# Optimization experiments

Hardware: AMD Instinct MI355X
Metric: run time of the kernel (lower is better)

## Reference

```python
import jax, jax.numpy as jnp
import numpy as np

B, L, H, D = 64, 2048, 1024, 128  # segments, segment length, hidden, input_dim
N = B * L

def swish(z):
    return z * jax.nn.sigmoid(z)

def setup_inputs() -> dict:
    key = jax.random.key(0)
    ks = jax.random.split(key, 10)
    s = 0.02
    x_seeds = jax.random.normal(ks[0], (N, D), dtype=jnp.float32)
    x_nodes = jax.random.normal(ks[1], (N, D), dtype=jnp.float32)
    W_seed = jax.random.normal(ks[2], (H, D), dtype=jnp.float32) * s
    W_node = jax.random.normal(ks[3], (H, D), dtype=jnp.float32) * s
    W1 = jax.random.normal(ks[4], (H, H), dtype=jnp.float32) * s
    b1 = jnp.zeros((H,), dtype=jnp.float32)
    W2 = jax.random.normal(ks[5], (H, H), dtype=jnp.float32) * s
    b2 = jnp.zeros((H,), dtype=jnp.float32)
    w_ns = jax.random.normal(ks[6], (1, H), dtype=jnp.float32) * s   # node_score_layer (zero-init in src; random for nontrivial baseline)
    W_stop = jax.random.normal(ks[7], (2, H), dtype=jnp.float32) * s  # stopping_score_layer
    starts = jnp.arange(B, dtype=jnp.int32) * L
    indptr = jnp.stack([starts, starts + L, starts + L], axis=1)  # (start, end, candidate_end)
    return {"x_seeds": x_seeds, "x_nodes": x_nodes, "W_seed": W_seed, "W_node": W_node,
            "W1": W1, "b1": b1, "W2": W2, "b2": b2, "w_ns": w_ns, "W_stop": W_stop,
            "indptr": indptr}

def reference(x_seeds, x_nodes, W_seed, W_node, W1, b1, W2, b2, w_ns, W_stop, indptr):
    # embeddings + 2-layer Swish MLP
    h = x_seeds @ W_seed.T + x_nodes @ W_node.T            # [N, H]
    h = swish(h @ W1.T + b1)
    h = swish(h @ W2.T + b2)
    node_scores = (h @ w_ns.T)[:, 0]                       # [N]
    # ragged segments (uniform length L) defined by indptr starts
    nb = indptr.shape[0]
    seg_len = h.shape[0] // nb                             # static L
    idx = indptr[:, 0][:, None] + jnp.arange(seg_len)      # [B, L]
    h_seg = h[idx]                                         # [B, L, H]
    stop_node = h_seg.mean(axis=1)                         # [B, H] per-segment mean pool
    node_logits = jax.nn.log_softmax(node_scores[idx], axis=1)          # [B, L]
    stop_logits = jax.nn.log_softmax(stop_node @ W_stop.T, axis=1)      # [B, 2]
    # concat([node_logits + stop0, stop1]) per segment
    return jnp.concatenate([node_logits + stop_logits[:, :1], stop_logits[:, 1:]], axis=1)  # [B, L+1]
```

## Files before the change

kernel.cpp:

```cpp
#include <hip/hip_runtime.h>

typedef float f32x4 __attribute__((ext_vector_type(4)));
typedef __bf16 bf16x8 __attribute__((ext_vector_type(8)));
typedef unsigned short u16x8 __attribute__((ext_vector_type(8)));

#define DEVINL static __device__ __forceinline__

DEVINL unsigned short f2bf(float f) {
    unsigned int u = __builtin_bit_cast(unsigned int, f);
    u += 0x7fffu + ((u >> 16) & 1u);
    return (unsigned short)(u >> 16);
}
DEVINL float bf2f(unsigned short u) {
    unsigned int x = ((unsigned int)u) << 16;
    return __builtin_bit_cast(float, x);
}

#define GLD16(gp, lp)                                                          \
    __builtin_amdgcn_global_load_lds(                                          \
        (const __attribute__((address_space(1))) void*)(gp),                   \
        (__attribute__((address_space(3))) void*)(lp), 16, 0, 0)

__global__ void pack_cat_k(const float* __restrict__ s0, const float* __restrict__ s1,
                           unsigned short* __restrict__ dst, int nchunks) {
    int e = blockIdx.x * 256 + threadIdx.x;
    if (e >= nchunks) return;
    int row = e >> 5, ch = e & 31;
    const float* src = (ch < 16) ? (s0 + (size_t)row * 128 + ch * 8)
                                 : (s1 + (size_t)row * 128 + (ch - 16) * 8);
    float4 a = *(const float4*)src;
    float4 b = *(const float4*)(src + 4);
    u16x8 o;
    o[0] = f2bf(a.x); o[1] = f2bf(a.y); o[2] = f2bf(a.z); o[3] = f2bf(a.w);
    o[4] = f2bf(b.x); o[5] = f2bf(b.y); o[6] = f2bf(b.z); o[7] = f2bf(b.w);
    *(u16x8*)(dst + (size_t)e * 8) = o;
}

__global__ void cvt_k(const float* __restrict__ s, unsigned short* __restrict__ d, int nchunks) {
    int e = blockIdx.x * 256 + threadIdx.x;
    if (e >= nchunks) return;
    float4 a = *(const float4*)(s + (size_t)e * 8);
    float4 b = *(const float4*)(s + (size_t)e * 8 + 4);
    u16x8 o;
    o[0] = f2bf(a.x); o[1] = f2bf(a.y); o[2] = f2bf(a.z); o[3] = f2bf(a.w);
    o[4] = f2bf(b.x); o[5] = f2bf(b.y); o[6] = f2bf(b.z); o[7] = f2bf(b.w);
    *(u16x8*)(d + (size_t)e * 8) = o;
}

template <int EPI>
__global__ void gemm_bt_k(const unsigned short* __restrict__ A,
                          const unsigned short* __restrict__ B,
                          const float* __restrict__ bias,
                          unsigned short* __restrict__ C,
                          int M, int N, int K) {
    __shared__ unsigned short As[128 * 32];
    __shared__ unsigned short Bs[128 * 32];
    const int tid  = threadIdx.x;
    const int lane = tid & 63;
    const int wv   = tid >> 6;
    const int wr   = wv >> 1, wc = wv & 1;
    const int ntn  = N >> 7;
    const int im   = blockIdx.x / ntn, in = blockIdx.x % ntn;
    const size_t rowA0 = (size_t)im * 128, rowB0 = (size_t)in * 128;

    const int e0 = tid, e1 = tid + 256;
    const int ra0 = e0 >> 2, ca0 = (e0 & 3) * 8;
    const int ra1 = e1 >> 2, ca1 = (e1 & 3) * 8;

    f32x4 acc[4][4] = {};

    const int frow = lane & 15;
    const int kb   = (lane >> 4) * 8;

    for (int k0 = 0; k0 < K; k0 += 32) {
        GLD16(A + (rowA0 + ra0) * K + k0 + ca0, (char*)As + e0 * 16);
        GLD16(A + (rowA0 + ra1) * K + k0 + ca1, (char*)As + e1 * 16);
        GLD16(B + (rowB0 + ra0) * K + k0 + ca0, (char*)Bs + e0 * 16);
        GLD16(B + (rowB0 + ra1) * K + k0 + ca1, (char*)Bs + e1 * 16);
        __syncthreads();

        bf16x8 af[4], bfr[4];
#pragma unroll
        for (int m = 0; m < 4; ++m)
            af[m] = *(const bf16x8*)&As[(wr * 64 + m * 16 + frow) * 32 + kb];
#pragma unroll
        for (int n = 0; n < 4; ++n)
            bfr[n] = *(const bf16x8*)&Bs[(wc * 64 + n * 16 + frow) * 32 + kb];
#pragma unroll
        for (int m = 0; m < 4; ++m)
#pragma unroll
            for (int n = 0; n < 4; ++n)
                acc[m][n] = __builtin_amdgcn_mfma_f32_16x16x32_bf16(af[m], bfr[n], acc[m][n], 0, 0, 0);
        __syncthreads();
    }

    const int r4 = (lane >> 4) * 4;
    const int cc = lane & 15;
#pragma unroll
    for (int n = 0; n < 4; ++n) {
        const int col = (int)rowB0 + wc * 64 + n * 16 + cc;
        const float bv = (EPI == 1) ? bias[col] : 0.0f;
#pragma unroll
        for (int m = 0; m < 4; ++m) {
            const size_t row = rowA0 + wr * 64 + m * 16 + r4;
#pragma unroll
            for (int r = 0; r < 4; ++r) {
                float v = acc[m][n][r] + bv;
                if (EPI == 1) v = v / (1.0f + __expf(-v));
                C[(row + r) * (size_t)N + col] = f2bf(v);
            }
        }
    }
}

__global__ void scores_k(const unsigned short* __restrict__ h,
                         const float* __restrict__ wns, float* __restrict__ sc) {
    const int lane = threadIdx.x & 63, wv = threadIdx.x >> 6;
    const size_t row = (size_t)blockIdx.x * 4 + wv;
    const unsigned short* p = h + row * 1024;
    float s = 0.f;
#pragma unroll
    for (int it = 0; it < 2; ++it) {
        const int base = (it * 64 + lane) * 8;
        u16x8 v = *(const u16x8*)&p[base];
        const float4 w0 = *(const float4*)&wns[base];
        const float4 w1 = *(const float4*)&wns[base + 4];
        s += bf2f(v[0]) * w0.x + bf2f(v[1]) * w0.y + bf2f(v[2]) * w0.z + bf2f(v[3]) * w0.w
           + bf2f(v[4]) * w1.x + bf2f(v[5]) * w1.y + bf2f(v[6]) * w1.z + bf2f(v[7]) * w1.w;
    }
#pragma unroll
    for (int off = 32; off; off >>= 1) s += __shfl_down(s, off);
    if (lane == 0) sc[row] = s;
}

__global__ void pool_k(const unsigned short* __restrict__ h, float* __restrict__ pool) {
    const int bi = blockIdx.x;
    const int b = bi >> 5, sub = bi & 31;
    const int rb = sub >> 2, cb = sub & 3;
    const int hc = cb * 256 + threadIdx.x;
    const unsigned short* p = h + ((size_t)b * 2048 + rb * 256) * 1024 + hc;
    float acc = 0.f;
#pragma unroll 8
    for (int r = 0; r < 256; ++r) acc += bf2f(p[(size_t)r * 1024]);
    atomicAdd(&pool[b * 1024 + hc], acc * (1.0f / 2048.0f));
}

__global__ void stop_k(const float* __restrict__ pool, const float* __restrict__ Wstop,
                       float* __restrict__ stp, float* __restrict__ out) {
    const int b = blockIdx.x, t = threadIdx.x;
    float a0 = 0.f, a1 = 0.f;
#pragma unroll
    for (int j = 0; j < 4; ++j) {
        const int hcol = t + j * 256;
        const float pv = pool[b * 1024 + hcol];
        a0 += pv * Wstop[hcol];
        a1 += pv * Wstop[1024 + hcol];
    }
    const int lane = t & 63, wv = t >> 6;
#pragma unroll
    for (int off = 32; off; off >>= 1) { a0 += __shfl_down(a0, off); a1 += __shfl_down(a1, off); }
    __shared__ float r0[4], r1[4];
    if (lane == 0) { r0[wv] = a0; r1[wv] = a1; }
    __syncthreads();
    if (t == 0) {
        const float s0 = r0[0] + r0[1] + r0[2] + r0[3];
        const float s1 = r1[0] + r1[1] + r1[2] + r1[3];
        const float m  = fmaxf(s0, s1);
        const float lse = m + __logf(__expf(s0 - m) + __expf(s1 - m));
        stp[b * 2] = s0 - lse;
        out[(size_t)b * 2049 + 2048] = s1 - lse;
    }
}

__global__ void node_k(const float* __restrict__ sc, const float* __restrict__ stp,
                       float* __restrict__ out) {
    const int b = blockIdx.x, t = threadIdx.x;
    const float* s = sc + (size_t)b * 2048;
    float v[8];
    float mx = -3.4e38f;
#pragma unroll
    for (int j = 0; j < 8; ++j) { v[j] = s[t + j * 256]; mx = fmaxf(mx, v[j]); }
    const int lane = t & 63, wv = t >> 6;
    __shared__ float red[4];
#pragma unroll
    for (int off = 32; off; off >>= 1) mx = fmaxf(mx, __shfl_down(mx, off));
    if (lane == 0) red[wv] = mx;
    __syncthreads();
    mx = fmaxf(fmaxf(red[0], red[1]), fmaxf(red[2], red[3]));
    float se = 0.f;
#pragma unroll
    for (int j = 0; j < 8; ++j) se += __expf(v[j] - mx);
    __syncthreads();
#pragma unroll
    for (int off = 32; off; off >>= 1) se += __shfl_down(se, off);
    if (lane == 0) red[wv] = se;
    __syncthreads();
    se = red[0] + red[1] + red[2] + red[3];
    const float base = stp[b * 2] - mx - __logf(se);
#pragma unroll
    for (int j = 0; j < 8; ++j) out[(size_t)b * 2049 + t + j * 256] = v[j] + base;
}

extern "C" void kernel_launch(void* const* d_in, const int* in_sizes, int n_in,
                              void* d_out, int out_size, void* d_ws, size_t ws_size,
                              hipStream_t stream) {
    (void)in_sizes; (void)n_in; (void)out_size;
    const float* x_seeds = (const float*)d_in[0];
    const float* x_nodes = (const float*)d_in[1];
    const float* W_seed  = (const float*)d_in[2];
    const float* W_node  = (const float*)d_in[3];
    const float* W1      = (const float*)d_in[4];
    const float* b1      = (const float*)d_in[5];
    const float* W2      = (const float*)d_in[6];
    const float* b2      = (const float*)d_in[7];
    const float* w_ns    = (const float*)d_in[8];
    const float* W_stop  = (const float*)d_in[9];
    float* out = (float*)d_out;

    const int N = 131072, H = 1024, B = 64;

    char* ws = (char*)d_ws;
    size_t off = 0;
    auto alloc = [&](size_t bytes) {
        char* p = ws + off;
        off += (bytes + 255) & ~(size_t)255;
        return p;
    };
    unsigned short* wcat = (unsigned short*)alloc((size_t)H * 256 * 2);
    unsigned short* W1b  = (unsigned short*)alloc((size_t)H * H * 2);
    unsigned short* W2b  = (unsigned short*)alloc((size_t)H * H * 2);
    float* scores = (float*)alloc((size_t)N * 4);
    float* pool   = (float*)alloc((size_t)B * H * 4);
    float* stp    = (float*)alloc((size_t)B * 2 * 4);

    const size_t per_row = 256 * 2 + 1024 * 2 + 1024 * 2;
    size_t avail = (ws_size > off + (1u << 20)) ? (ws_size - off - (1u << 20)) : 0;
    long long mc_ll = (long long)(avail / per_row) / 2048 * 2048;
    int Mc = (int)(mc_ll < 2048 ? 2048 : (mc_ll > 65536 ? 65536 : mc_ll));

    unsigned short* xcat_c = (unsigned short*)alloc((size_t)Mc * 256 * 2);
    unsigned short* h0_c   = (unsigned short*)alloc((size_t)Mc * H * 2);
    unsigned short* h1_c   = (unsigned short*)alloc((size_t)Mc * H * 2);

    hipMemsetAsync(pool, 0, (size_t)B * H * 4, stream);

    pack_cat_k<<<(H * 32) / 256, 256, 0, stream>>>(W_seed, W_node, wcat, H * 32);
    cvt_k<<<(H * H / 8) / 256, 256, 0, stream>>>(W1, W1b, H * H / 8);
    cvt_k<<<(H * H / 8) / 256, 256, 0, stream>>>(W2, W2b, H * H / 8);

    for (int base = 0; base < N; base += Mc) {
        const int m = (N - base < Mc) ? (N - base) : Mc;
        pack_cat_k<<<(m * 32) / 256, 256, 0, stream>>>(
            x_seeds + (size_t)base * 128, x_nodes + (size_t)base * 128, xcat_c, m * 32);
        const int grid = (m / 128) * (H / 128);
        gemm_bt_k<0><<<grid, 256, 0, stream>>>(xcat_c, wcat, nullptr, h0_c, m, H, 256);
        gemm_bt_k<1><<<grid, 256, 0, stream>>>(h0_c, W1b, b1, h1_c, m, H, H);
        gemm_bt_k<1><<<grid, 256, 0, stream>>>(h1_c, W2b, b2, h0_c, m, H, H);
        scores_k<<<m / 4, 256, 0, stream>>>(h0_c, w_ns, scores + base);
        pool_k<<<(m / 2048) * 32, 256, 0, stream>>>(h0_c, pool + (size_t)(base / 2048) * H);
    }

    stop_k<<<B, 256, 0, stream>>>(pool, W_stop, stp, out);
    node_k<<<B, 256, 0, stream>>>(scores, stp, out);
}
```

Baseline: 1.247 ms.

## Fuse score and mean-pool reductions into final GEMM epilogue, add XCD-aware block remap

The last MLP GEMM now applies bias and swish, then computes per-row node scores with lane shuffles and per-column segment sums directly from the accumulators, using atomics. This removes writing the final hidden activations to memory and the separate scores and pool kernels that read them back. Block indices are also remapped so that consecutive logical tiles land on the same XCD, which is meant to improve L2 reuse. The cost is float atomics on scores, which now need a memset, and nondeterministic summation order.

Measured after the change: 1.013 ms. 18.8% less time.

```diff
diff --git a/kernel.cpp b/kernel.cpp
--- a/kernel.cpp
+++ b/kernel.cpp
@@ -52,6 +52,9 @@
                           const unsigned short* __restrict__ B,
                           const float* __restrict__ bias,
                           unsigned short* __restrict__ C,
+                          const float* __restrict__ wns,
+                          float* __restrict__ sc,
+                          float* __restrict__ pl,
                           int M, int N, int K) {
     __shared__ unsigned short As[128 * 32];
     __shared__ unsigned short Bs[128 * 32];
@@ -60,7 +63,13 @@
     const int wv   = tid >> 6;
     const int wr   = wv >> 1, wc = wv & 1;
     const int ntn  = N >> 7;
-    const int im   = blockIdx.x / ntn, in = blockIdx.x % ntn;
+
+    const int nwg = gridDim.x;
+    const int xcd = blockIdx.x & 7, blk = blockIdx.x >> 3;
+    const int q = nwg >> 3, rr = nwg & 7;
+    const int logical = (xcd < rr ? xcd * (q + 1) : rr * (q + 1) + (xcd - rr) * q) + blk;
+
+    const int im   = logical / ntn, in = logical % ntn;
     const size_t rowA0 = (size_t)im * 128, rowB0 = (size_t)in * 128;
 
     const int e0 = tid, e1 = tid + 256;
@@ -96,6 +105,49 @@
 
     const int r4 = (lane >> 4) * 4;
     const int cc = lane & 15;
+
+    if (EPI == 2) {
+#pragma unroll
+        for (int n = 0; n < 4; ++n) {
+            const float bv = bias[(int)rowB0 + wc * 64 + n * 16 + cc];
+#pragma unroll
+            for (int m = 0; m < 4; ++m)
+#pragma unroll
+                for (int r = 0; r < 4; ++r) {
+                    float v = acc[m][n][r] + bv;
+                    acc[m][n][r] = v / (1.0f + __expf(-v));
+                }
+        }
+#pragma unroll
+        for (int m = 0; m < 4; ++m)
+#pragma unroll
+            for (int r = 0; r < 4; ++r) {
+                float s = 0.f;
+#pragma unroll
+                for (int n = 0; n < 4; ++n)
+                    s += acc[m][n][r] * wns[(int)rowB0 + wc * 64 + n * 16 + cc];
+#pragma unroll
+                for (int o = 1; o < 16; o <<= 1) s += __shfl_xor(s, o);
+                if (cc == 0)
+                    atomicAdd(&sc[rowA0 + wr * 64 + m * 16 + r4 + r], s);
+            }
+        const int seg = (int)(rowA0 >> 11);
+#pragma unroll
+        for (int n = 0; n < 4; ++n) {
+            float p = 0.f;
+#pragma unroll
+            for (int m = 0; m < 4; ++m)
+#pragma unroll
+                for (int r = 0; r < 4; ++r) p += acc[m][n][r];
+            p += __shfl_xor(p, 16);
+            p += __shfl_xor(p, 32);
+            if ((lane >> 4) == 0)
+                atomicAdd(&pl[seg * 1024 + (int)rowB0 + wc * 64 + n * 16 + cc],
+                          p * (1.0f / 2048.0f));
+        }
+        return;
+    }
+
 #pragma unroll
     for (int n = 0; n < 4; ++n) {
         const int col = (int)rowB0 + wc * 64 + n * 16 + cc;
@@ -111,38 +163,6 @@
             }
         }
     }
-}
-
-__global__ void scores_k(const unsigned short* __restrict__ h,
-                         const float* __restrict__ wns, float* __restrict__ sc) {
-    const int lane = threadIdx.x & 63, wv = threadIdx.x >> 6;
-    const size_t row = (size_t)blockIdx.x * 4 + wv;
-    const unsigned short* p = h + row * 1024;
-    float s = 0.f;
-#pragma unroll
-    for (int it = 0; it < 2; ++it) {
-        const int base = (it * 64 + lane) * 8;
-        u16x8 v = *(const u16x8*)&p[base];
-        const float4 w0 = *(const float4*)&wns[base];
-        const float4 w1 = *(const float4*)&wns[base + 4];
-        s += bf2f(v[0]) * w0.x + bf2f(v[1]) * w0.y + bf2f(v[2]) * w0.z + bf2f(v[3]) * w0.w
-           + bf2f(v[4]) * w1.x + bf2f(v[5]) * w1.y + bf2f(v[6]) * w1.z + bf2f(v[7]) * w1.w;
-    }
-#pragma unroll
-    for (int off = 32; off; off >>= 1) s += __shfl_down(s, off);
-    if (lane == 0) sc[row] = s;
-}
-
-__global__ void pool_k(const unsigned short* __restrict__ h, float* __restrict__ pool) {
-    const int bi = blockIdx.x;
-    const int b = bi >> 5, sub = bi & 31;
-    const int rb = sub >> 2, cb = sub & 3;
-    const int hc = cb * 256 + threadIdx.x;
-    const unsigned short* p = h + ((size_t)b * 2048 + rb * 256) * 1024 + hc;
-    float acc = 0.f;
-#pragma unroll 8
-    for (int r = 0; r < 256; ++r) acc += bf2f(p[(size_t)r * 1024]);
-    atomicAdd(&pool[b * 1024 + hc], acc * (1.0f / 2048.0f));
 }
 
 __global__ void stop_k(const float* __restrict__ pool, const float* __restrict__ Wstop,
@@ -243,6 +263,7 @@
     unsigned short* h1_c   = (unsigned short*)alloc((size_t)Mc * H * 2);
 
     hipMemsetAsync(pool, 0, (size_t)B * H * 4, stream);
+    hipMemsetAsync(scores, 0, (size_t)N * 4, stream);
 
     pack_cat_k<<<(H * 32) / 256, 256, 0, stream>>>(W_seed, W_node, wcat, H * 32);
     cvt_k<<<(H * H / 8) / 256, 256, 0, stream>>>(W1, W1b, H * H / 8);
@@ -253,11 +274,13 @@
         pack_cat_k<<<(m * 32) / 256, 256, 0, stream>>>(
             x_seeds + (size_t)base * 128, x_nodes + (size_t)base * 128, xcat_c, m * 32);
         const int grid = (m / 128) * (H / 128);
-        gemm_bt_k<0><<<grid, 256, 0, stream>>>(xcat_c, wcat, nullptr, h0_c, m, H, 256);
-        gemm_bt_k<1><<<grid, 256, 0, stream>>>(h0_c, W1b, b1, h1_c, m, H, H);
-        gemm_bt_k<1><<<grid, 256, 0, stream>>>(h1_c, W2b, b2, h0_c, m, H, H);
-        scores_k<<<m / 4, 256, 0, stream>>>(h0_c, w_ns, scores + base);
-        pool_k<<<(m / 2048) * 32, 256, 0, stream>>>(h0_c, pool + (size_t)(base / 2048) * H);
+        gemm_bt_k<0><<<grid, 256, 0, stream>>>(xcat_c, wcat, nullptr, h0_c,
+                                               nullptr, nullptr, nullptr, m, H, 256);
+        gemm_bt_k<1><<<grid, 256, 0, stream>>>(h0_c, W1b, b1, h1_c,
+                                               nullptr, nullptr, nullptr, m, H, H);
+        gemm_bt_k<2><<<grid, 256, 0, stream>>>(h1_c, W2b, b2, nullptr,
+                                               w_ns, scores + base,
+                                               pool + (size_t)(base / 2048) * H, m, H, H);
     }
 
     stop_k<<<B, 256, 0, stream>>>(pool, W_stop, stp, out);
```
